# Optimization experiments

Measured on AMD Instinct MI355X. Metric: run time of the kernel, lower is better.

The kernel has to match this reference:

```python
import jax, jax.numpy as jnp
import numpy as np

SPARSITY_A = 0.1
SPARSITY_B = 0.5

N, L, C = 8, 8192, 3


def setup_inputs() -> dict:
    key = jax.random.key(0)
    k1, k2, k3, k4 = jax.random.split(key, 4)
    inp = jax.random.normal(k1, (N, L, C), dtype=jnp.float32)
    tgt = jax.random.uniform(k2, (N, L, C), dtype=jnp.float32)
    class_weights = jax.random.uniform(k3, (C,), dtype=jnp.float32) + 0.5
    pos_weight = jax.random.uniform(k4, (C,), dtype=jnp.float32) * 4.0 + 1.0
    return {"input": inp, "target": tgt, "class_weights": class_weights, "pos_weight": pos_weight}


def _proximity(s1, s2):
    # full cross-correlation (length 2L-1), same set of values as torch conv1d w/ padding=L-1
    cc = jnp.convolve(s1, s2[::-1], mode="full")
    e1 = jnp.sum(s1 * s1)
    e2 = jnp.sum(s2 * s2)
    norm = jnp.sqrt(e1 * e2)
    penalty = 1.0 - jnp.sqrt(e1 + e2) / norm
    return (cc / norm + penalty).mean()


def _sparsity(x):
    # NOTE: original code does x[1:] - x[:1] (diff vs FIRST element), preserved here.
    # x: (N, L, C-1) -> (N, C-1)
    d = x[:, 1:, :] - x[:, :1, :]
    return SPARSITY_A * jnp.sum(jnp.abs(d) - SPARSITY_B * jnp.maximum(d, 0.0), axis=1)


def reference(input, target, class_weights, pos_weight):
    # --- weighted BCE-with-logits per channel ---
    log_sig = jax.nn.log_sigmoid(input)      # (N,L,C)
    log_one_minus = jax.nn.log_sigmoid(-input)
    bce = -(pos_weight * target * log_sig + (1.0 - target) * log_one_minus)
    bce_per_c = bce.mean(axis=(0, 1))        # (C,)
    loss = jnp.sum(10.0 * class_weights * bce_per_c)

    # --- proximity between channels 1 and 2, per batch element ---
    prox = jax.vmap(_proximity)(input[:, :, 1], input[:, :, 2])  # (N,)
    loss = loss + jnp.sum(prox)

    # --- sparsity loss over channels 1..C-1, per batch element ---
    s_in = _sparsity(input[:, :, 1:])    # (N, C-1)
    s_tg = _sparsity(target[:, :, 1:])   # (N, C-1)
    loss = loss + jnp.sum(jnp.abs(s_in - s_tg) / (s_tg + 1.0))
    return loss
```

## Files before the change

### kernel.cpp

```cpp
#include <hip/hip_runtime.h>
#include <math.h>

#define LEN 8192
#define NBATCH 8
#define NCH 3
#define BLK 256
#define PPT 4
#define BPN (LEN / (BLK * PPT))
#define NBLOCKS (NBATCH * BPN)
#define NQ 11


__device__ __forceinline__ float log_sigmoid(float x) {
    return fminf(x, 0.0f) - log1pf(expf(-fabsf(x)));
}

__device__ __forceinline__ float sp_term(float d) {
    return fabsf(d) - 0.5f * fmaxf(d, 0.0f);
}

__global__ __launch_bounds__(BLK) void fused_kernel(
        const float* __restrict__ inp,
        const float* __restrict__ tgt,
        const float* __restrict__ cw,
        const float* __restrict__ pw,
        unsigned int* __restrict__ counter,
        float* __restrict__ part,
        float* __restrict__ out) {
    const int b = blockIdx.x;
    const int n = b >> 3;
    const int l0 = (((b & 7) << 8) + threadIdx.x) * PPT;
    const float* ip = inp + (size_t)n * LEN * NCH;
    const float* tp = tgt + (size_t)n * LEN * NCH;

    const float bi1 = ip[1], bi2 = ip[2];
    const float bt1 = tp[1], bt2 = tp[2];
    const float pw0 = pw[0], pw1 = pw[1], pw2 = pw[2];

    const float4* i4 = reinterpret_cast<const float4*>(ip + (size_t)l0 * NCH);
    const float4* t4 = reinterpret_cast<const float4*>(tp + (size_t)l0 * NCH);
    const float4 ia = i4[0], ib = i4[1], ic = i4[2];
    const float4 ta = t4[0], tb = t4[1], tc = t4[2];

    const float xs[PPT][3] = {{ia.x, ia.y, ia.z}, {ia.w, ib.x, ib.y},
                              {ib.z, ib.w, ic.x}, {ic.y, ic.z, ic.w}};
    const float tss[PPT][3] = {{ta.x, ta.y, ta.z}, {ta.w, tb.x, tb.y},
                               {tb.z, tb.w, tc.x}, {tc.y, tc.z, tc.w}};

    float v[NQ];
#pragma unroll
    for (int q = 0; q < NQ; ++q) v[q] = 0.0f;

#pragma unroll
    for (int p = 0; p < PPT; ++p) {
        const float x0 = xs[p][0], x1 = xs[p][1], x2 = xs[p][2];
        const float t0 = tss[p][0], t1 = tss[p][1], t2 = tss[p][2];
        v[0] += (1.0f - t0) * x0 - (pw0 * t0 + 1.0f - t0) * log_sigmoid(x0);
        v[1] += (1.0f - t1) * x1 - (pw1 * t1 + 1.0f - t1) * log_sigmoid(x1);
        v[2] += (1.0f - t2) * x2 - (pw2 * t2 + 1.0f - t2) * log_sigmoid(x2);
        v[3] += x1;
        v[4] += x2;
        v[5] += x1 * x1;
        v[6] += x2 * x2;
        v[7]  += sp_term(x1 - bi1);
        v[8]  += sp_term(x2 - bi2);
        v[9]  += sp_term(t1 - bt1);
        v[10] += sp_term(t2 - bt2);
    }

    __shared__ float red[4][NQ];
    const int lane = threadIdx.x & 63;
    const int wv   = threadIdx.x >> 6;
#pragma unroll
    for (int q = 0; q < NQ; ++q) {
        float s = v[q];
#pragma unroll
        for (int off = 32; off >= 1; off >>= 1) s += __shfl_down(s, off, 64);
        if (lane == 0) red[wv][q] = s;
    }
    __syncthreads();

    __shared__ int lastFlag;
    if (threadIdx.x == 0) {
#pragma unroll
        for (int q = 0; q < NQ; ++q)
            part[b * NQ + q] = red[0][q] + red[1][q] + red[2][q] + red[3][q];
        __threadfence();
        unsigned int old = atomicAdd(counter, 1u);
        lastFlag = (old == NBLOCKS - 1);
    }
    __syncthreads();
    if (!lastFlag) return;

    __threadfence();
    __shared__ float bceS[3];
    __shared__ float perN[NBATCH][8];
    if (threadIdx.x < 64) {
        volatile const float* vp = part + threadIdx.x * NQ;
        float r[NQ];
#pragma unroll
        for (int q = 0; q < NQ; ++q) r[q] = vp[q];
#pragma unroll
        for (int q = 0; q < 3; ++q) {
            float s = r[q];
#pragma unroll
            for (int off = 32; off >= 1; off >>= 1) s += __shfl_down(s, off, 64);
            if (threadIdx.x == 0) bceS[q] = s;
        }
#pragma unroll
        for (int q = 3; q < NQ; ++q) {
            float s = r[q];
#pragma unroll
            for (int off = 4; off >= 1; off >>= 1) s += __shfl_down(s, off, 8);
            if ((threadIdx.x & 7) == 0) perN[threadIdx.x >> 3][q - 3] = s;
        }
    }
    __syncthreads();

    if (threadIdx.x == 0) {
        float loss = 0.0f;
        const float invNL = 1.0f / (float)(NBATCH * LEN);
#pragma unroll
        for (int c = 0; c < 3; ++c)
            loss += 10.0f * cw[c] * (bceS[c] * invNL);
#pragma unroll
        for (int n2 = 0; n2 < NBATCH; ++n2) {
            const float sum1 = perN[n2][0], sum2 = perN[n2][1];
            const float e1   = perN[n2][2], e2   = perN[n2][3];
            const float norm = sqrtf(e1 * e2);
            loss += (sum1 * sum2) / (norm * (float)(2 * LEN - 1))
                    + 1.0f - sqrtf(e1 + e2) / norm;
#pragma unroll
            for (int c = 0; c < 2; ++c) {
                const float si = 0.1f * perN[n2][4 + c];
                const float st = 0.1f * perN[n2][6 + c];
                loss += fabsf(si - st) / (st + 1.0f);
            }
        }
        out[0] = loss;
    }
}

extern "C" void kernel_launch(void* const* d_in, const int* in_sizes, int n_in,
                              void* d_out, int out_size, void* d_ws, size_t ws_size,
                              hipStream_t stream) {
    const float* inp = (const float*)d_in[0];
    const float* tgt = (const float*)d_in[1];
    const float* cw  = (const float*)d_in[2];
    const float* pw  = (const float*)d_in[3];

    unsigned int* counter = (unsigned int*)d_ws;
    float* part = (float*)((char*)d_ws + 256);

    hipMemsetAsync(counter, 0, sizeof(unsigned int), stream);
    fused_kernel<<<NBLOCKS, BLK, 0, stream>>>(inp, tgt, cw, pw,
                                              counter, part, (float*)d_out);
}
```

Before: 73.46 us.

## Split fused last-block reduction into partial and finalize kernels with wave-sized blocks

Replaces the single fused kernel, which used an atomic counter and a last-block-done pattern, with two launches: a partial-sum kernel of 256 single-wave blocks and a one-wave finalize kernel. This drops the memset, the atomics, the threadfences and the shared-memory cross-wave reduction. The cost is a second kernel launch and a dependency between the two kernels, in exchange for more blocks and no LDS syncs.

```diff
diff --git a/kernel.cpp b/kernel.cpp
--- a/kernel.cpp
+++ b/kernel.cpp
@@ -4,9 +4,9 @@
 #define LEN 8192
 #define NBATCH 8
 #define NCH 3
-#define BLK 256
+#define ABLK 64
 #define PPT 4
-#define BPN (LEN / (BLK * PPT))
+#define BPN (LEN / (ABLK * PPT))
 #define NBLOCKS (NBATCH * BPN)
 #define NQ 11
 
@@ -19,17 +19,14 @@
     return fabsf(d) - 0.5f * fmaxf(d, 0.0f);
 }
 
-__global__ __launch_bounds__(BLK) void fused_kernel(
+__global__ __launch_bounds__(ABLK) void partial_kernel(
         const float* __restrict__ inp,
         const float* __restrict__ tgt,
-        const float* __restrict__ cw,
         const float* __restrict__ pw,
-        unsigned int* __restrict__ counter,
-        float* __restrict__ part,
-        float* __restrict__ out) {
+        float* __restrict__ part) {
     const int b = blockIdx.x;
-    const int n = b >> 3;
-    const int l0 = (((b & 7) << 8) + threadIdx.x) * PPT;
+    const int n = b >> 5;
+    const int l0 = (((b & 31) << 6) + threadIdx.x) * PPT;
     const float* ip = inp + (size_t)n * LEN * NCH;
     const float* tp = tgt + (size_t)n * LEN * NCH;
 
@@ -42,8 +39,8 @@
     const float4 ia = i4[0], ib = i4[1], ic = i4[2];
     const float4 ta = t4[0], tb = t4[1], tc = t4[2];
 
-    const float xs[PPT][3] = {{ia.x, ia.y, ia.z}, {ia.w, ib.x, ib.y},
-                              {ib.z, ib.w, ic.x}, {ic.y, ic.z, ic.w}};
+    const float xs[PPT][3]  = {{ia.x, ia.y, ia.z}, {ia.w, ib.x, ib.y},
+                               {ib.z, ib.w, ic.x}, {ic.y, ic.z, ic.w}};
     const float tss[PPT][3] = {{ta.x, ta.y, ta.z}, {ta.w, tb.x, tb.y},
                                {tb.z, tb.w, tc.x}, {tc.y, tc.z, tc.w}};
 
@@ -68,76 +65,66 @@
         v[10] += sp_term(t2 - bt2);
     }
 
-    __shared__ float red[4][NQ];
-    const int lane = threadIdx.x & 63;
-    const int wv   = threadIdx.x >> 6;
 #pragma unroll
     for (int q = 0; q < NQ; ++q) {
         float s = v[q];
 #pragma unroll
         for (int off = 32; off >= 1; off >>= 1) s += __shfl_down(s, off, 64);
-        if (lane == 0) red[wv][q] = s;
+        v[q] = s;
     }
-    __syncthreads();
-
-    __shared__ int lastFlag;
     if (threadIdx.x == 0) {
 #pragma unroll
-        for (int q = 0; q < NQ; ++q)
-            part[b * NQ + q] = red[0][q] + red[1][q] + red[2][q] + red[3][q];
-        __threadfence();
-        unsigned int old = atomicAdd(counter, 1u);
-        lastFlag = (old == NBLOCKS - 1);
+        for (int q = 0; q < NQ; ++q) part[b * NQ + q] = v[q];
     }
-    __syncthreads();
-    if (!lastFlag) return;
+}
 
-    __threadfence();
-    __shared__ float bceS[3];
-    __shared__ float perN[NBATCH][8];
-    if (threadIdx.x < 64) {
-        volatile const float* vp = part + threadIdx.x * NQ;
-        float r[NQ];
+__global__ __launch_bounds__(64) void finalize_kernel(
+        const float* __restrict__ part,
+        const float* __restrict__ cw,
+        float* __restrict__ out) {
+    const int lane = threadIdx.x;
+    float r[NQ];
 #pragma unroll
-        for (int q = 0; q < NQ; ++q) r[q] = vp[q];
+    for (int q = 0; q < NQ; ++q) {
+        const float* p = part + (lane * 4) * NQ + q;
+        r[q] = p[0] + p[NQ] + p[2 * NQ] + p[3 * NQ];
+    }
+
+    float bce0 = r[0], bce1 = r[1], bce2 = r[2];
 #pragma unroll
-        for (int q = 0; q < 3; ++q) {
-            float s = r[q];
+    for (int off = 32; off >= 1; off >>= 1) {
+        bce0 += __shfl_down(bce0, off, 64);
+        bce1 += __shfl_down(bce1, off, 64);
+        bce2 += __shfl_down(bce2, off, 64);
+    }
+
 #pragma unroll
-            for (int off = 32; off >= 1; off >>= 1) s += __shfl_down(s, off, 64);
-            if (threadIdx.x == 0) bceS[q] = s;
-        }
+    for (int q = 3; q < NQ; ++q) {
 #pragma unroll
-        for (int q = 3; q < NQ; ++q) {
-            float s = r[q];
+        for (int off = 4; off >= 1; off >>= 1) r[q] += __shfl_down(r[q], off, 8);
+    }
+
+    float c = 0.0f;
+    if ((lane & 7) == 0) {
+        const float sum1 = r[3], sum2 = r[4];
+        const float e1 = r[5], e2 = r[6];
+        const float norm = sqrtf(e1 * e2);
+        c = (sum1 * sum2) / (norm * (float)(2 * LEN - 1))
+            + 1.0f - sqrtf(e1 + e2) / norm;
 #pragma unroll
-            for (int off = 4; off >= 1; off >>= 1) s += __shfl_down(s, off, 8);
-            if ((threadIdx.x & 7) == 0) perN[threadIdx.x >> 3][q - 3] = s;
+        for (int ch = 0; ch < 2; ++ch) {
+            const float si = 0.1f * r[7 + ch];
+            const float st = 0.1f * r[9 + ch];
+            c += fabsf(si - st) / (st + 1.0f);
         }
     }
-    __syncthreads();
+#pragma unroll
+    for (int off = 32; off >= 1; off >>= 1) c += __shfl_down(c, off, 64);
 
-    if (threadIdx.x == 0) {
-        float loss = 0.0f;
+    if (lane == 0) {
         const float invNL = 1.0f / (float)(NBATCH * LEN);
-#pragma unroll
-        for (int c = 0; c < 3; ++c)
-            loss += 10.0f * cw[c] * (bceS[c] * invNL);
-#pragma unroll
-        for (int n2 = 0; n2 < NBATCH; ++n2) {
-            const float sum1 = perN[n2][0], sum2 = perN[n2][1];
-            const float e1   = perN[n2][2], e2   = perN[n2][3];
-            const float norm = sqrtf(e1 * e2);
-            loss += (sum1 * sum2) / (norm * (float)(2 * LEN - 1))
-                    + 1.0f - sqrtf(e1 + e2) / norm;
-#pragma unroll
-            for (int c = 0; c < 2; ++c) {
-                const float si = 0.1f * perN[n2][4 + c];
-                const float st = 0.1f * perN[n2][6 + c];
-                loss += fabsf(si - st) / (st + 1.0f);
-            }
-        }
-        out[0] = loss;
+        float loss = 10.0f * (cw[0] * bce0 + cw[1] * bce1 + cw[2] * bce2) * invNL;
+        out[0] = loss + c;
     }
 }
 
@@ -148,11 +135,8 @@
     const float* tgt = (const float*)d_in[1];
     const float* cw  = (const float*)d_in[2];
     const float* pw  = (const float*)d_in[3];
+    float* part = (float*)d_ws;
 
-    unsigned int* counter = (unsigned int*)d_ws;
-    float* part = (float*)((char*)d_ws + 256);
-
-    hipMemsetAsync(counter, 0, sizeof(unsigned int), stream);
-    fused_kernel<<<NBLOCKS, BLK, 0, stream>>>(inp, tgt, cw, pw,
-                                              counter, part, (float*)d_out);
+    partial_kernel<<<NBLOCKS, ABLK, 0, stream>>>(inp, tgt, pw, part);
+    finalize_kernel<<<1, 64, 0, stream>>>(part, cw, (float*)d_out);
 }
```

After: 65.58 us. -10.7%, faster.
